# Performance work log

Hardware: AMD Instinct MI355X
Metric: run time of the kernel (lower is better)

Reference implementation:

```python
import jax, jax.numpy as jnp
import numpy as np

NUM_GROUPS = 32
EPS = 1e-6


def group_norm(x, gamma, beta):
    # x: [b, c, t, h, w]
    b, c, t, h, w = x.shape
    xg = x.reshape(b, NUM_GROUPS, c // NUM_GROUPS, t, h, w)
    mean = xg.mean(axis=(2, 3, 4, 5), keepdims=True)
    var = xg.var(axis=(2, 3, 4, 5), keepdims=True)
    xg = (xg - mean) * jax.lax.rsqrt(var + EPS)
    xn = xg.reshape(b, c, t, h, w)
    return xn * gamma[None, :, None, None, None] + beta[None, :, None, None, None]


def conv1x1(x, w, bias):
    # 1x1x1 Conv3d == per-position channel matmul. x: [b,c,t,h,w], w: [cout,cin]
    y = jnp.einsum('oc,bcthw->bothw', w, x)
    return y + bias[None, :, None, None, None]


def setup_inputs() -> dict:
    key = jax.random.key(0)
    ks = jax.random.split(key, 11)
    c = 512
    b, t, h, w = 1, 16, 32, 32
    s = 1.0 / np.sqrt(c)
    return {
        'x': jax.random.normal(ks[0], (b, c, t, h, w), dtype=jnp.float32),
        'gn_gamma': jnp.ones((c,), jnp.float32),
        'gn_beta': jnp.zeros((c,), jnp.float32),
        'wq': jax.random.normal(ks[1], (c, c), jnp.float32) * s,
        'bq': jnp.zeros((c,), jnp.float32),
        'wk': jax.random.normal(ks[2], (c, c), jnp.float32) * s,
        'bk': jnp.zeros((c,), jnp.float32),
        'wv': jax.random.normal(ks[3], (c, c), jnp.float32) * s,
        'bv': jnp.zeros((c,), jnp.float32),
        'wo': jax.random.normal(ks[4], (c, c), jnp.float32) * s,
        'bo': jnp.zeros((c,), jnp.float32),
    }


def reference(x, gn_gamma, gn_beta, wq, bq, wk, bk, wv, bv, wo, bo):
    b, c, t, h, w = x.shape
    h_ = group_norm(x, gn_gamma, gn_beta)
    q = conv1x1(h_, wq, bq)
    k = conv1x1(h_, wk, bk)
    v = conv1x1(h_, wv, bv)
    # per-frame spatial attention: tokens are the h*w grid, batched over (b t)
    n = h * w
    q = q.transpose(0, 2, 3, 4, 1).reshape(b * t, n, c)   # [(bt), n, c]
    k = k.transpose(0, 2, 3, 4, 1).reshape(b * t, n, c)
    v = v.transpose(0, 2, 3, 4, 1).reshape(b * t, n, c)
    scale = float(int(c) ** (-0.5))
    attn = jax.nn.softmax(jnp.einsum('bic,bjc->bij', q, k) * scale, axis=-1)
    out = jnp.einsum('bij,bjc->bic', attn, v)             # [(bt), n, c]
    out = out.reshape(b, t, h, w, c).transpose(0, 4, 1, 2, 3)
    out = conv1x1(out, wo, bo)
    return x + out
```

## Files before the change

### kernel.cpp

```cpp
#include <hip/hip_runtime.h>
#include <hip/hip_bf16.h>

#define CCH   512
#define NPOS  16384
#define NTOK  1024
#define NFRM  16
#define NGRP  32
#define GSZ   (CCH / NGRP)
#define GELEM (GSZ * NPOS)
#define GN_SPLIT 32

typedef unsigned short u16;
typedef unsigned int   u32;
typedef __attribute__((ext_vector_type(8))) short  short8;
typedef __attribute__((ext_vector_type(4))) float  floatx4;

__device__ __forceinline__ float bf2f(u16 u) {
    return __uint_as_float(((u32)u) << 16);
}
__device__ __forceinline__ u16 f2bf(float f) {
    u32 u = __float_as_uint(f);
    u = (u + 0x7fffu + ((u >> 16) & 1u)) >> 16;
    return (u16)u;
}
__device__ __forceinline__ float ldx(const void* p, size_t i, bool f32m) {
    return f32m ? ((const float*)p)[i] : bf2f(((const u16*)p)[i]);
}
__device__ __forceinline__ void gl2lds16(const u16* g, u16* l) {
    __builtin_amdgcn_global_load_lds(
        (const __attribute__((address_space(1))) u32*)g,
        (__attribute__((address_space(3))) u32*)l, 16, 0, 0);
}

__launch_bounds__(256)
__global__ void detect_dtype(const u32* __restrict__ x32, u32* __restrict__ flag) {
    __shared__ int cnt;
    if (threadIdx.x == 0) cnt = 0;
    __syncthreads();
    int c = 0;
    for (int i = threadIdx.x; i < 4096; i += 256) {
        u32 v = x32[i] & 0xFFFFu;
        u32 e = (v >> 7) & 0xFFu;
        if (e >= 0xC8u) c++;
    }
    atomicAdd(&cnt, c);
    __syncthreads();
    if (threadIdx.x == 0) *flag = (cnt > 64) ? 1u : 0u;
}

__launch_bounds__(256)
__global__ void conv_all(const void* w0, const void* w1, const void* w2, const void* w3,
                         const void* b0, const void* b1, const void* b2, const void* b3,
                         u16* __restrict__ wdst, u16* __restrict__ bdst,
                         const u32* __restrict__ flag) {
    bool f32m = *flag != 0u;
    int b = blockIdx.x;
    if (b < 1024) {
        int wi = b >> 8;
        const void* src = (wi == 0) ? w0 : (wi == 1) ? w1 : (wi == 2) ? w2 : w3;
        int base = (b & 255) * 1024 + threadIdx.x * 4;
        u16* d = wdst + wi * 262144 + base;
        if (f32m) {
            float4 v = *(const float4*)((const float*)src + base);
            ushort4 o;
            o.x = f2bf(v.x); o.y = f2bf(v.y); o.z = f2bf(v.z); o.w = f2bf(v.w);
            *(ushort4*)d = o;
        } else {
            *(ushort4*)d = *(const ushort4*)((const u16*)src + base);
        }
    } else {
        int t = threadIdx.x;
        int bi = t >> 6;
        int off = (t & 63) * 8;
        const void* src = (bi == 0) ? b0 : (bi == 1) ? b1 : (bi == 2) ? b2 : b3;
        u16* d = bdst + bi * 512 + off;
        if (f32m) {
            float4 v1 = *(const float4*)((const float*)src + off);
            float4 v2 = *(const float4*)((const float*)src + off + 4);
            ushort4 o1, o2;
            o1.x = f2bf(v1.x); o1.y = f2bf(v1.y); o1.z = f2bf(v1.z); o1.w = f2bf(v1.w);
            o2.x = f2bf(v2.x); o2.y = f2bf(v2.y); o2.z = f2bf(v2.z); o2.w = f2bf(v2.w);
            *(ushort4*)d = o1; *(ushort4*)(d + 4) = o2;
        } else {
            *(ushort4*)d = *(const ushort4*)((const u16*)src + off);
            *(ushort4*)(d + 4) = *(const ushort4*)((const u16*)src + off + 4);
        }
    }
}

__launch_bounds__(256)
__global__ void zero_rl(float* __restrict__ rl) {
    rl[blockIdx.x * 256 + threadIdx.x] = 0.0f;
}

__launch_bounds__(256)
__global__ void gn_partial(const void* __restrict__ x, float2* __restrict__ partials,
                           const u32* __restrict__ flag) {
    __shared__ float sm[8];
    bool f32m = *flag != 0u;
    const int chunk = GELEM / GN_SPLIT;
    size_t base = (size_t)blockIdx.x * chunk;
    float s = 0.f, ss = 0.f;
    if (f32m) {
        const float4* p = (const float4*)((const float*)x + base);
        for (int i = threadIdx.x; i < chunk / 4; i += 256) {
            float4 u = p[i];
            s  += u.x + u.y + u.z + u.w;
            ss += u.x * u.x + u.y * u.y + u.z * u.z + u.w * u.w;
        }
    } else {
        const ushort4* p = (const ushort4*)((const u16*)x + base);
        for (int i = threadIdx.x; i < chunk / 4; i += 256) {
            ushort4 u = p[i];
            float a = bf2f(u.x), b = bf2f(u.y), c = bf2f(u.z), d = bf2f(u.w);
            s  += a + b + c + d;
            ss += a * a + b * b + c * c + d * d;
        }
    }
    int lane = threadIdx.x & 63, w = threadIdx.x >> 6;
    float t = s;
    #pragma unroll
    for (int o = 32; o > 0; o >>= 1) t += __shfl_down(t, o, 64);
    if (lane == 0) sm[w] = t;
    t = ss;
    #pragma unroll
    for (int o = 32; o > 0; o >>= 1) t += __shfl_down(t, o, 64);
    if (lane == 0) sm[4 + w] = t;
    __syncthreads();
    if (threadIdx.x == 0)
        partials[blockIdx.x] = make_float2(sm[0] + sm[1] + sm[2] + sm[3],
                                           sm[4] + sm[5] + sm[6] + sm[7]);
}

__launch_bounds__(256)
__global__ void gn_coef(const float2* __restrict__ partials, const void* __restrict__ gamma,
                        const void* __restrict__ beta, float2* __restrict__ coef,
                        const u32* __restrict__ flag) {
    bool f32m = *flag != 0u;
    int c = blockIdx.x * 256 + threadIdx.x;
    if (c < CCH) {
        int g = c >> 4;
        float sum = 0.f, sq = 0.f;
        #pragma unroll
        for (int i = 0; i < GN_SPLIT; ++i) {
            float2 p = partials[g * GN_SPLIT + i];
            sum += p.x; sq += p.y;
        }
        float mean = sum * (1.0f / (float)GELEM);
        float var  = fmaxf(sq * (1.0f / (float)GELEM) - mean * mean, 0.0f);
        float rstd = rsqrtf(var + 1e-6f);
        float gm = ldx(gamma, c, f32m), b = ldx(beta, c, f32m);
        float sc = rstd * gm;
        coef[c] = make_float2(sc, b - mean * sc);
    }
}

__launch_bounds__(256)
__global__ void gn_apply_t(const void* __restrict__ x, const float2* __restrict__ coef,
                           u16* __restrict__ xt, const u32* __restrict__ flag) {
    bool f32m = *flag != 0u;
    __shared__ float tile[64][65];
    int p0 = blockIdx.x * 64, c0 = blockIdx.y * 64;
    int lane = threadIdx.x & 63, rg = threadIdx.x >> 6;
    #pragma unroll 4
    for (int i = 0; i < 16; ++i) {
        int row = rg * 16 + i;
        int c = c0 + row;
        float2 cf = coef[c];
        float v = ldx(x, (size_t)c * NPOS + p0 + lane, f32m);
        tile[row][lane] = v * cf.x + cf.y;
    }
    __syncthreads();
    #pragma unroll 4
    for (int i = 0; i < 16; ++i) {
        int prow = rg * 16 + i;
        xt[(size_t)(p0 + prow) * CCH + c0 + lane] = f2bf(tile[lane][prow]);
    }
}

#define EPI_QK    0
#define EPI_V     1
#define EPI_SCEXP 2
#define EPI_PV    3
#define EPI_OUT   4

template<int EPI, bool MX, bool FSW>
__launch_bounds__(256)
__global__ void mfma_gemm(const u16* __restrict__ A, const u16* __restrict__ B,
                          void* __restrict__ C, const u16* __restrict__ bias,
                          const void* __restrict__ resid, const u32* __restrict__ flag,
                          float* __restrict__ rl,
                          int lda, int ldb, int ldc, int K,
                          long aFS, long bFS, long cFS) {
    __shared__ __align__(16) u16 As[128 * 32];
    __shared__ __align__(16) u16 Bs[128 * 32];
    const int tid = threadIdx.x;

    int bxi, byi, f;
    if (FSW) {
        u32 id = (blockIdx.z * gridDim.y + blockIdx.y) * gridDim.x + blockIdx.x;
        u32 T = gridDim.x * gridDim.y * gridDim.z;
        u32 half = T >> 1;
        f = (int)(id & 7u) + ((id >= half) ? 8 : 0);
        u32 l = (id >= half ? id - half : id) >> 3;
        bxi = (int)(l % gridDim.x);
        byi = (int)(l / gridDim.x);
    } else {
        bxi = blockIdx.x; byi = blockIdx.y; f = blockIdx.z;
    }
    const int m_blk = MX ? bxi : byi;
    const int n_blk = MX ? byi : bxi;

    const u16* Ab = A + (size_t)f * aFS + (size_t)m_blk * 128 * lda;
    const u16* Bb = B + (size_t)f * bFS + (size_t)n_blk * 128 * ldb;

    const int wave = tid >> 6, lane = tid & 63;
    const int srow = wave * 32 + (lane >> 2);
    const int sch  = (lane & 3) * 8;
    u16* lA0 = &As[wave * 1024];
    u16* lA1 = &As[wave * 1024 + 512];
    u16* lB0 = &Bs[wave * 1024];
    u16* lB1 = &Bs[wave * 1024 + 512];

    const int wm = (wave >> 1) * 64, wn = (wave & 1) * 64;
    const int l15 = lane & 15, quad = lane >> 4;

    floatx4 acc[4][4] = {};

    for (int kk = 0; kk < K; kk += 32) {
        __syncthreads();
        gl2lds16(Ab + (size_t)srow * lda + kk + sch,        lA0);
        gl2lds16(Ab + (size_t)(srow + 16) * lda + kk + sch, lA1);
        gl2lds16(Bb + (size_t)srow * ldb + kk + sch,        lB0);
        gl2lds16(Bb + (size_t)(srow + 16) * ldb + kk + sch, lB1);
        __syncthreads();
        short8 af[4], bf[4];
        #pragma unroll
        for (int mi = 0; mi < 4; ++mi)
            af[mi] = *(const short8*)&As[(wm + mi * 16 + l15) * 32 + quad * 8];
        #pragma unroll
        for (int ni = 0; ni < 4; ++ni)
            bf[ni] = *(const short8*)&Bs[(wn + ni * 16 + l15) * 32 + quad * 8];
        #pragma unroll
        for (int mi = 0; mi < 4; ++mi)
            #pragma unroll
            for (int ni = 0; ni < 4; ++ni)
                acc[mi][ni] = __builtin_amdgcn_mfma_f32_16x16x32_bf16(
                    af[mi], bf[ni], acc[mi][ni], 0, 0, 0);
    }

    const bool f32m = (EPI == EPI_OUT) ? (*flag != 0u) : false;
    const int m_base = m_blk * 128 + wm;
    const int n_base = n_blk * 128 + wn;
    const float scale = 0.044194173824159216f;

    float inv[4][4];
    if (EPI == EPI_PV) {
        #pragma unroll
        for (int mi = 0; mi < 4; ++mi)
            #pragma unroll
            for (int r = 0; r < 4; ++r)
                inv[mi][r] = 1.0f / rl[f * NTOK + m_base + mi * 16 + quad * 4 + r];
    }
    float rs[4][4];
    if (EPI == EPI_SCEXP) {
        #pragma unroll
        for (int mi = 0; mi < 4; ++mi)
            #pragma unroll
            for (int r = 0; r < 4; ++r) rs[mi][r] = 0.0f;
    }

    #pragma unroll
    for (int mi = 0; mi < 4; ++mi) {
        #pragma unroll
        for (int ni = 0; ni < 4; ++ni) {
            int n = n_base + ni * 16 + l15;
            float bn = (EPI == EPI_QK) ? bf2f(bias[n]) : 0.0f;
            #pragma unroll
            for (int r = 0; r < 4; ++r) {
                int m = m_base + mi * 16 + quad * 4 + r;
                float v = acc[mi][ni][r];
                size_t idx = (size_t)f * cFS + (size_t)m * ldc + n;
                if (EPI == EPI_QK) {
                    ((u16*)C)[idx] = f2bf(v + bn);
                } else if (EPI == EPI_V) {
                    ((u16*)C)[idx] = f2bf(v + bf2f(bias[m]));
                } else if (EPI == EPI_SCEXP) {
                    float ex = __expf(v * scale);
                    rs[mi][r] += ex;
                    ((u16*)C)[idx] = f2bf(ex);
                } else if (EPI == EPI_PV) {
                    ((u16*)C)[idx] = f2bf(v * inv[mi][r]);
                } else {
                    float r2 = v + bf2f(bias[m]) + ldx(resid, idx, f32m);
                    if (f32m) ((float*)C)[idx] = r2;
                    else      ((u16*)C)[idx]   = f2bf(r2);
                }
            }
        }
    }

    if (EPI == EPI_SCEXP) {
        #pragma unroll
        for (int mi = 0; mi < 4; ++mi) {
            #pragma unroll
            for (int r = 0; r < 4; ++r) {
                float s = rs[mi][r];
                s += __shfl_xor(s, 1, 64);
                s += __shfl_xor(s, 2, 64);
                s += __shfl_xor(s, 4, 64);
                s += __shfl_xor(s, 8, 64);
                if (l15 == 0)
                    atomicAdd(&rl[f * NTOK + m_base + mi * 16 + quad * 4 + r], s);
            }
        }
    }
}

extern "C" void kernel_launch(void* const* d_in, const int* in_sizes, int n_in,
                              void* d_out, int out_size, void* d_ws, size_t ws_size,
                              hipStream_t stream) {
    const void* x   = d_in[0];
    const void* gam = d_in[1];
    const void* bet = d_in[2];

    char* ws = (char*)d_ws;
    float2* coef     = (float2*)(ws);
    float2* partials = (float2*)(ws + 4096);
    u32*    flag     = (u32*)(ws + 12352);
    u16* cw[4] = { (u16*)(ws + 16384),              (u16*)(ws + 16384 +  524288ull),
                   (u16*)(ws + 16384 + 1048576ull), (u16*)(ws + 16384 + 1572864ull) };
    u16* cb[4] = { (u16*)(ws + 2113536ull),        (u16*)(ws + 2113536ull + 1024),
                   (u16*)(ws + 2113536ull + 2048), (u16*)(ws + 2113536ull + 3072) };
    float* rl  = (float*)(ws + (3ull << 20));
    u16*  xnt  = (u16*)(ws + (4ull  << 20));
    u16*  qt   = (u16*)(ws + (20ull << 20));
    u16*  kt   = (u16*)(ws + (36ull << 20));
    u16*  vt   = (u16*)(ws + (52ull << 20));
    u16*  pbuf = (u16*)(ws + (68ull << 20));
    u16*  obuf = xnt;

    detect_dtype<<<1, 256, 0, stream>>>((const u32*)x, flag);
    conv_all<<<1025, 256, 0, stream>>>(d_in[3], d_in[5], d_in[7], d_in[9],
                                       d_in[4], d_in[6], d_in[8], d_in[10],
                                       cw[0], cb[0], flag);
    gn_partial<<<NGRP * GN_SPLIT, 256, 0, stream>>>(x, partials, flag);
    gn_coef<<<2, 256, 0, stream>>>(partials, gam, bet, coef, flag);
    gn_apply_t<<<dim3(NPOS / 64, CCH / 64), 256, 0, stream>>>(x, coef, xnt, flag);
    zero_rl<<<NPOS / 256, 256, 0, stream>>>(rl);

    dim3 gqk(NPOS / 128, CCH / 128, 1);
    mfma_gemm<EPI_QK, true, false><<<gqk, 256, 0, stream>>>(
        xnt, cw[0], qt, cb[0], nullptr, flag, nullptr, CCH, CCH, CCH, CCH, 0, 0, 0);
    mfma_gemm<EPI_QK, true, false><<<gqk, 256, 0, stream>>>(
        xnt, cw[1], kt, cb[1], nullptr, flag, nullptr, CCH, CCH, CCH, CCH, 0, 0, 0);
    dim3 gv(NPOS / 128, CCH / 128, 1);
    mfma_gemm<EPI_V, false, false><<<gv, 256, 0, stream>>>(
        cw[2], xnt, vt, cb[2], nullptr, flag, nullptr, CCH, CCH, NPOS, CCH, 0, 0, 0);

    dim3 gsc(NTOK / 128, NTOK / 128, NFRM);
    mfma_gemm<EPI_SCEXP, false, true><<<gsc, 256, 0, stream>>>(
        qt, kt, pbuf, nullptr, nullptr, flag, rl, CCH, CCH, NTOK, CCH,
        (long)NTOK * CCH, (long)NTOK * CCH, (long)NTOK * NTOK);

    dim3 gpv(CCH / 128, NTOK / 128, NFRM);
    mfma_gemm<EPI_PV, false, true><<<gpv, 256, 0, stream>>>(
        pbuf, vt, obuf, nullptr, nullptr, flag, rl, NTOK, NPOS, CCH, NTOK,
        (long)NTOK * NTOK, NTOK, (long)NTOK * CCH);

    dim3 go(NPOS / 128, CCH / 128, 1);
    mfma_gemm<EPI_OUT, false, false><<<go, 256, 0, stream>>>(
        cw[3], obuf, d_out, cb[3], x, flag, nullptr, CCH, CCH, NPOS, CCH, 0, 0, 0);
}
```

Baseline: 272.2 us.

## Widen GEMM K-tile to 64 with XOR-swizzled LDS and fuse Q/K projections

The shared MFMA GEMM now stages 64-wide K slices instead of 32, halving the number of barrier pairs per tile. It stores the slices in LDS with an XOR swizzle so fragment reads avoid bank conflicts, and requests 3 blocks per SIMD through launch bounds. The Q and K projections become one GEMM writing an interleaved [pos, 1024] buffer, which the score GEMM reads with a stride of 1024. The rl zeroing kernel is folded into the weight-conversion launch. Doubling the LDS tile to 32 KB per block and capping registers for occupancy could limit residency or cause spills.

```diff
diff --git a/kernel.cpp b/kernel.cpp
--- a/kernel.cpp
+++ b/kernel.cpp
@@ -52,9 +52,14 @@
 __global__ void conv_all(const void* w0, const void* w1, const void* w2, const void* w3,
                          const void* b0, const void* b1, const void* b2, const void* b3,
                          u16* __restrict__ wdst, u16* __restrict__ bdst,
+                         float* __restrict__ rl,
                          const u32* __restrict__ flag) {
+    int b = blockIdx.x;
+    if (b > 1024) {
+        rl[(b - 1025) * 256 + threadIdx.x] = 0.0f;
+        return;
+    }
     bool f32m = *flag != 0u;
-    int b = blockIdx.x;
     if (b < 1024) {
         int wi = b >> 8;
         const void* src = (wi == 0) ? w0 : (wi == 1) ? w1 : (wi == 2) ? w2 : w3;
@@ -89,11 +94,6 @@
 }
 
 __launch_bounds__(256)
-__global__ void zero_rl(float* __restrict__ rl) {
-    rl[blockIdx.x * 256 + threadIdx.x] = 0.0f;
-}
-
-__launch_bounds__(256)
 __global__ void gn_partial(const void* __restrict__ x, float2* __restrict__ partials,
                            const u32* __restrict__ flag) {
     __shared__ float sm[8];
@@ -185,15 +185,15 @@
 #define EPI_OUT   4
 
 template<int EPI, bool MX, bool FSW>
-__launch_bounds__(256)
+__launch_bounds__(256, 3)
 __global__ void mfma_gemm(const u16* __restrict__ A, const u16* __restrict__ B,
                           void* __restrict__ C, const u16* __restrict__ bias,
                           const void* __restrict__ resid, const u32* __restrict__ flag,
                           float* __restrict__ rl,
                           int lda, int ldb, int ldc, int K,
                           long aFS, long bFS, long cFS) {
-    __shared__ __align__(16) u16 As[128 * 32];
-    __shared__ __align__(16) u16 Bs[128 * 32];
+    __shared__ __align__(16) u16 As[128 * 64];
+    __shared__ __align__(16) u16 Bs[128 * 64];
     const int tid = threadIdx.x;
 
     int bxi, byi, f;
@@ -215,38 +215,44 @@
     const u16* Bb = B + (size_t)f * bFS + (size_t)n_blk * 128 * ldb;
 
     const int wave = tid >> 6, lane = tid & 63;
-    const int srow = wave * 32 + (lane >> 2);
-    const int sch  = (lane & 3) * 8;
-    u16* lA0 = &As[wave * 1024];
-    u16* lA1 = &As[wave * 1024 + 512];
-    u16* lB0 = &Bs[wave * 1024];
-    u16* lB1 = &Bs[wave * 1024 + 512];
+    const int srow8 = wave * 32 + (lane >> 3);
+    const int schs  = ((lane & 7) ^ ((lane >> 3) & 7)) * 8;
+    u16* lA = &As[wave * 2048];
+    u16* lB = &Bs[wave * 2048];
 
     const int wm = (wave >> 1) * 64, wn = (wave & 1) * 64;
     const int l15 = lane & 15, quad = lane >> 4;
 
     floatx4 acc[4][4] = {};
 
-    for (int kk = 0; kk < K; kk += 32) {
+    for (int kk = 0; kk < K; kk += 64) {
         __syncthreads();
-        gl2lds16(Ab + (size_t)srow * lda + kk + sch,        lA0);
-        gl2lds16(Ab + (size_t)(srow + 16) * lda + kk + sch, lA1);
-        gl2lds16(Bb + (size_t)srow * ldb + kk + sch,        lB0);
-        gl2lds16(Bb + (size_t)(srow + 16) * ldb + kk + sch, lB1);
+        #pragma unroll
+        for (int o = 0; o < 4; ++o) {
+            gl2lds16(Ab + (size_t)(srow8 + o * 8) * lda + kk + schs, lA + o * 512);
+            gl2lds16(Bb + (size_t)(srow8 + o * 8) * ldb + kk + schs, lB + o * 512);
+        }
         __syncthreads();
-        short8 af[4], bf[4];
-        #pragma unroll
-        for (int mi = 0; mi < 4; ++mi)
-            af[mi] = *(const short8*)&As[(wm + mi * 16 + l15) * 32 + quad * 8];
-        #pragma unroll
-        for (int ni = 0; ni < 4; ++ni)
-            bf[ni] = *(const short8*)&Bs[(wn + ni * 16 + l15) * 32 + quad * 8];
-        #pragma unroll
-        for (int mi = 0; mi < 4; ++mi)
-            #pragma unroll
-            for (int ni = 0; ni < 4; ++ni)
-                acc[mi][ni] = __builtin_amdgcn_mfma_f32_16x16x32_bf16(
-                    af[mi], bf[ni], acc[mi][ni], 0, 0, 0);
+        #pragma unroll
+        for (int kh = 0; kh < 2; ++kh) {
+            short8 af[4], bf[4];
+            #pragma unroll
+            for (int mi = 0; mi < 4; ++mi) {
+                const int row = wm + mi * 16 + l15;
+                af[mi] = *(const short8*)&As[row * 64 + (((kh << 2) | quad) ^ (row & 7)) * 8];
+            }
+            #pragma unroll
+            for (int ni = 0; ni < 4; ++ni) {
+                const int row = wn + ni * 16 + l15;
+                bf[ni] = *(const short8*)&Bs[row * 64 + (((kh << 2) | quad) ^ (row & 7)) * 8];
+            }
+            #pragma unroll
+            for (int mi = 0; mi < 4; ++mi)
+                #pragma unroll
+                for (int ni = 0; ni < 4; ++ni)
+                    acc[mi][ni] = __builtin_amdgcn_mfma_f32_16x16x32_bf16(
+                        af[mi], bf[ni], acc[mi][ni], 0, 0, 0);
+        }
     }
 
     const bool f32m = (EPI == EPI_OUT) ? (*flag != 0u) : false;
@@ -334,34 +340,30 @@
                    (u16*)(ws + 2113536ull + 2048), (u16*)(ws + 2113536ull + 3072) };
     float* rl  = (float*)(ws + (3ull << 20));
     u16*  xnt  = (u16*)(ws + (4ull  << 20));
-    u16*  qt   = (u16*)(ws + (20ull << 20));
-    u16*  kt   = (u16*)(ws + (36ull << 20));
+    u16*  qkt  = (u16*)(ws + (20ull << 20));
     u16*  vt   = (u16*)(ws + (52ull << 20));
     u16*  pbuf = (u16*)(ws + (68ull << 20));
     u16*  obuf = xnt;
 
     detect_dtype<<<1, 256, 0, stream>>>((const u32*)x, flag);
-    conv_all<<<1025, 256, 0, stream>>>(d_in[3], d_in[5], d_in[7], d_in[9],
+    conv_all<<<1089, 256, 0, stream>>>(d_in[3], d_in[5], d_in[7], d_in[9],
                                        d_in[4], d_in[6], d_in[8], d_in[10],
-                                       cw[0], cb[0], flag);
+                                       cw[0], cb[0], rl, flag);
     gn_partial<<<NGRP * GN_SPLIT, 256, 0, stream>>>(x, partials, flag);
     gn_coef<<<2, 256, 0, stream>>>(partials, gam, bet, coef, flag);
     gn_apply_t<<<dim3(NPOS / 64, CCH / 64), 256, 0, stream>>>(x, coef, xnt, flag);
-    zero_rl<<<NPOS / 256, 256, 0, stream>>>(rl);
-
-    dim3 gqk(NPOS / 128, CCH / 128, 1);
+
+    dim3 gqk(NPOS / 128, 1024 / 128, 1);
     mfma_gemm<EPI_QK, true, false><<<gqk, 256, 0, stream>>>(
-        xnt, cw[0], qt, cb[0], nullptr, flag, nullptr, CCH, CCH, CCH, CCH, 0, 0, 0);
-    mfma_gemm<EPI_QK, true, false><<<gqk, 256, 0, stream>>>(
-        xnt, cw[1], kt, cb[1], nullptr, flag, nullptr, CCH, CCH, CCH, CCH, 0, 0, 0);
+        xnt, cw[0], qkt, cb[0], nullptr, flag, nullptr, CCH, CCH, 1024, CCH, 0, 0, 0);
     dim3 gv(NPOS / 128, CCH / 128, 1);
     mfma_gemm<EPI_V, false, false><<<gv, 256, 0, stream>>>(
         cw[2], xnt, vt, cb[2], nullptr, flag, nullptr, CCH, CCH, NPOS, CCH, 0, 0, 0);
 
     dim3 gsc(NTOK / 128, NTOK / 128, NFRM);
     mfma_gemm<EPI_SCEXP, false, true><<<gsc, 256, 0, stream>>>(
-        qt, kt, pbuf, nullptr, nullptr, flag, rl, CCH, CCH, NTOK, CCH,
-        (long)NTOK * CCH, (long)NTOK * CCH, (long)NTOK * NTOK);
+        qkt, qkt + 512, pbuf, nullptr, nullptr, flag, rl, 1024, 1024, NTOK, CCH,
+        (long)NTOK * 1024, (long)NTOK * 1024, (long)NTOK * NTOK);
 
     dim3 gpv(CCH / 128, NTOK / 128, NFRM);
     mfma_gemm<EPI_PV, false, true><<<gpv, 256, 0, stream>>>(
```

After: 236.9 us. 12.9% less time.
